# Kernel optimization log

Hardware: AMD Instinct MI355X
Metric: run time of the kernel (lower is better)

Reference implementation:

```python
import jax, jax.numpy as jnp
import numpy as np

B, H, S, D = 4, 16, 2048, 64

def setup_inputs() -> dict:
    key = jax.random.key(0)
    kq, kk, kv = jax.random.split(key, 3)
    q = jax.random.normal(kq, (B, H, S, D), dtype=jnp.float32)
    k = jax.random.normal(kk, (B, H, S, D), dtype=jnp.float32)
    v = jax.random.normal(kv, (B, H, S, D), dtype=jnp.float32)
    return {"q": q, "k": k, "v": v}

def reference(q, k, v):
    # naive unfused attention: scores = QK^T / sqrt(d), softmax, then @ V
    scale = 1.0 / jnp.sqrt(jnp.asarray(q.shape[-1], q.dtype))
    scores = jnp.einsum('bhqd,bhkd->bhqk', q, k) * scale  # [B,H,S,S] materialized
    attn = jax.nn.softmax(scores, axis=-1)
    out = jnp.einsum('bhqk,bhkd->bhqd', attn, v)
    return out
```

## Files before the change

kernel.cpp:

```cpp
#include <hip/hip_runtime.h>


#define S_LEN 2048
#define D_DIM 64
#define N_BH  64
#define QSCALE 0.18033688011112042f

typedef _Float16 half8 __attribute__((ext_vector_type(8)));
typedef _Float16 half4 __attribute__((ext_vector_type(4)));
typedef float floatx16 __attribute__((ext_vector_type(16)));
typedef unsigned int uint4v __attribute__((ext_vector_type(4)));

#define MFMA32(a, b, c) __builtin_amdgcn_mfma_f32_32x32x16_f16((a), (b), (c), 0, 0, 0)

#define GLL16(g, l) __builtin_amdgcn_global_load_lds(                      \
    (const __attribute__((address_space(1))) void*)(g),                    \
    (__attribute__((address_space(3))) void*)(l), 16, 0, 0)

__global__ __launch_bounds__(256) void prep_kernel(
    const float* __restrict__ kg, const float* __restrict__ vg,
    _Float16* __restrict__ kh, _Float16* __restrict__ vt)
{
    __shared__ _Float16 Ls[64 * 64];
    const int tid = threadIdx.x;
    const int bh = blockIdx.y;
    const int sbase = blockIdx.x * 64;
    const size_t gbase = ((size_t)(bh * S_LEN + sbase)) * D_DIM;

#pragma unroll
    for (int i = 0; i < 4; ++i) {
        const int e = i * 1024 + tid * 4;
        const int s = e >> 6, d0 = e & 63;
        const float4 kv = *(const float4*)(kg + gbase + e);
        half4 hk;
        hk[0] = (_Float16)kv.x; hk[1] = (_Float16)kv.y;
        hk[2] = (_Float16)kv.z; hk[3] = (_Float16)kv.w;
        *(half4*)(kh + gbase + e) = hk;
        const float4 vv = *(const float4*)(vg + gbase + e);
        const int base = ((((s >> 3) ^ ((d0 >> 2) & 7)) << 3) | (s & 7));
        Ls[(d0 + 0) * 64 + base] = (_Float16)vv.x;
        Ls[(d0 + 1) * 64 + base] = (_Float16)vv.y;
        Ls[(d0 + 2) * 64 + base] = (_Float16)vv.z;
        Ls[(d0 + 3) * 64 + base] = (_Float16)vv.w;
    }
    __syncthreads();
    const int d = tid >> 2, c = tid & 3, sw = (d >> 2) & 7;
    _Float16* dst = vt + ((size_t)(bh * D_DIM + d)) * S_LEN + sbase + c * 16;
    *(half8*)(dst)     = *(const half8*)&Ls[d * 64 + (((2 * c)     ^ sw) << 3)];
    *(half8*)(dst + 8) = *(const half8*)&Ls[d * 64 + (((2 * c + 1) ^ sw) << 3)];
}

__global__ __launch_bounds__(128) void fa_kernel(
    const float* __restrict__ qg, const _Float16* __restrict__ kh,
    const _Float16* __restrict__ vt, float* __restrict__ outg)
{
    __shared__ _Float16 Kl[64 * 64];
    __shared__ _Float16 Vl[64 * 64];

    const int tid = threadIdx.x;
    const int w = tid >> 6;
    const int L = tid & 63;
    const int lq = L & 31;
    const int h = L >> 5;

    const int id = blockIdx.x;
    const int bh   = ((id & 7) << 3) | (id >> 8);
    const int qblk = (id >> 3) & 31;
    const int qrow = qblk * 64 + w * 32 + lq;

    half8 qb[4];
    {
        const float* qp = qg + ((size_t)bh * S_LEN + qrow) * D_DIM + h * 8;
#pragma unroll
        for (int ks = 0; ks < 4; ++ks) {
            const float4 a = *(const float4*)(qp + ks * 16);
            const float4 b = *(const float4*)(qp + ks * 16 + 4);
            qb[ks][0] = (_Float16)(a.x * QSCALE);
            qb[ks][1] = (_Float16)(a.y * QSCALE);
            qb[ks][2] = (_Float16)(a.z * QSCALE);
            qb[ks][3] = (_Float16)(a.w * QSCALE);
            qb[ks][4] = (_Float16)(b.x * QSCALE);
            qb[ks][5] = (_Float16)(b.y * QSCALE);
            qb[ks][6] = (_Float16)(b.z * QSCALE);
            qb[ks][7] = (_Float16)(b.w * QSCALE);
        }
    }

    floatx16 o0, o1, lac;
#pragma unroll
    for (int r = 0; r < 16; ++r) { o0[r] = 0.f; o1[r] = 0.f; lac[r] = 0.f; }

    half8 ones;
#pragma unroll
    for (int j = 0; j < 8; ++j) ones[j] = (_Float16)1.0f;

    const int rloc = L >> 3, lc = L & 7;
    const int crd = lc ^ rloc;
    const _Float16* kgl = kh + (size_t)bh * S_LEN * D_DIM
                        + (size_t)(w * 32 + rloc) * D_DIM + crd * 8;
    const _Float16* vgl = vt + (size_t)bh * D_DIM * S_LEN
                        + (size_t)(w * 32 + rloc) * S_LEN + crd * 8;
    _Float16* const kld = &Kl[w * 32 * 64];
    _Float16* const vld = &Vl[w * 32 * 64];

    for (int kt = 0; kt < S_LEN / 64; ++kt) {
        __syncthreads();
#pragma unroll
        for (int i = 0; i < 4; ++i) {
            GLL16(kgl + (size_t)i * 8 * D_DIM, kld + i * 8 * 64);
            GLL16(vgl + (size_t)i * 8 * S_LEN, vld + i * 8 * 64);
        }
        kgl += 64 * D_DIM;
        vgl += 64;
        __syncthreads();

        floatx16 sa0, sa1;
#pragma unroll
        for (int r = 0; r < 16; ++r) { sa0[r] = 0.f; sa1[r] = 0.f; }
#pragma unroll
        for (int ks = 0; ks < 4; ++ks) {
            const int sw = (((2 * ks + h) ^ (lq & 7)) << 3);
            const half8 ka0 = *(const half8*)&Kl[lq * 64 + sw];
            const half8 ka1 = *(const half8*)&Kl[(32 + lq) * 64 + sw];
            sa0 = MFMA32(ka0, qb[ks], sa0);
            sa1 = MFMA32(ka1, qb[ks], sa1);
        }

        unsigned int pk0[8], pk1[8];
#pragma unroll
        for (int p = 0; p < 8; ++p) {
            const auto e0 = __builtin_amdgcn_cvt_pkrtz(
                __builtin_amdgcn_exp2f(sa0[2 * p]),
                __builtin_amdgcn_exp2f(sa0[2 * p + 1]));
            const auto e1 = __builtin_amdgcn_cvt_pkrtz(
                __builtin_amdgcn_exp2f(sa1[2 * p]),
                __builtin_amdgcn_exp2f(sa1[2 * p + 1]));
            pk0[p] = __builtin_bit_cast(unsigned int, e0);
            pk1[p] = __builtin_bit_cast(unsigned int, e1);
        }

#pragma unroll
        for (int mt = 0; mt < 2; ++mt) {
            const unsigned int* pk = mt ? pk1 : pk0;
            const unsigned int t0 = h ? pk[0] : pk[2];
            const unsigned int t1 = h ? pk[1] : pk[3];
            const unsigned int t2 = h ? pk[4] : pk[6];
            const unsigned int t3 = h ? pk[5] : pk[7];
            const unsigned int r0 = __shfl_xor(t0, 32, 64);
            const unsigned int r1 = __shfl_xor(t1, 32, 64);
            const unsigned int r2 = __shfl_xor(t2, 32, 64);
            const unsigned int r3 = __shfl_xor(t3, 32, 64);
            uint4v u0, u1;
            if (h == 0) {
                u0[0] = pk[0]; u0[1] = pk[1]; u0[2] = r0; u0[3] = r1;
                u1[0] = pk[4]; u1[1] = pk[5]; u1[2] = r2; u1[3] = r3;
            } else {
                u0[0] = r0; u0[1] = r1; u0[2] = pk[2]; u0[3] = pk[3];
                u1[0] = r2; u1[1] = r3; u1[2] = pk[6]; u1[3] = pk[7];
            }
            const half8 af0 = __builtin_bit_cast(half8, u0);
            const half8 af1 = __builtin_bit_cast(half8, u1);
#pragma unroll
            for (int kl = 0; kl < 2; ++kl) {
                const int ksg = mt * 2 + kl;
                const half8 af = kl ? af1 : af0;
                const int sw = (((2 * ksg + h) ^ (lq & 7)) << 3);
                const half8 vb0 = *(const half8*)&Vl[lq * 64 + sw];
                const half8 vb1 = *(const half8*)&Vl[(32 + lq) * 64 + sw];
                lac = MFMA32(af, ones, lac);
                o0 = MFMA32(af, vb0, o0);
                o1 = MFMA32(af, vb1, o1);
            }
        }
    }

    float* ob = outg + ((size_t)bh * S_LEN + qblk * 64 + w * 32) * D_DIM;
#pragma unroll
    for (int reg = 0; reg < 16; ++reg) {
        const int q = (reg & 3) + 8 * (reg >> 2) + 4 * h;
        const float inv = 1.0f / lac[reg];
        ob[(size_t)q * D_DIM + lq]      = o0[reg] * inv;
        ob[(size_t)q * D_DIM + 32 + lq] = o1[reg] * inv;
    }
}

extern "C" void kernel_launch(void* const* d_in, const int* in_sizes, int n_in,
                              void* d_out, int out_size, void* d_ws, size_t ws_size,
                              hipStream_t stream) {
    const float* q = (const float*)d_in[0];
    const float* k = (const float*)d_in[1];
    const float* v = (const float*)d_in[2];
    float* out = (float*)d_out;
    (void)in_sizes; (void)n_in; (void)out_size; (void)ws_size;

    _Float16* kh = (_Float16*)d_ws;
    _Float16* vt = kh + (size_t)N_BH * S_LEN * D_DIM;

    prep_kernel<<<dim3(S_LEN / 64, N_BH), dim3(256), 0, stream>>>(k, v, kh, vt);
    fa_kernel<<<dim3(2048), dim3(128), 0, stream>>>(q, kh, vt, out);
}
```

Before: 246.5 us.

## Process two query tiles per wave and halve row-sum MFMAs

Each wave now computes 64 query rows as two 32-row tiles, so every K and V fragment read from LDS feeds twice as many MFMAs. The block grows to 4 waves covering 256 query rows, and the grid shrinks to 512 blocks. The softmax denominator now takes one MFMA against a ones vector on the fp16 sum of the two P fragments, instead of two MFMAs. In exchange, register pressure roughly doubles, fewer waves are resident per CU, and the row sums are accumulated partly in fp16.

```diff
diff --git a/kernel.cpp b/kernel.cpp
--- a/kernel.cpp
+++ b/kernel.cpp
@@ -8,6 +8,7 @@
 
 typedef _Float16 half8 __attribute__((ext_vector_type(8)));
 typedef _Float16 half4 __attribute__((ext_vector_type(4)));
+typedef _Float16 half2v __attribute__((ext_vector_type(2)));
 typedef float floatx16 __attribute__((ext_vector_type(16)));
 typedef unsigned int uint4v __attribute__((ext_vector_type(4)));
 
@@ -50,7 +51,7 @@
     *(half8*)(dst + 8) = *(const half8*)&Ls[d * 64 + (((2 * c + 1) ^ sw) << 3)];
 }
 
-__global__ __launch_bounds__(128) void fa_kernel(
+__global__ __launch_bounds__(256) void fa_kernel(
     const float* __restrict__ qg, const _Float16* __restrict__ kh,
     const _Float16* __restrict__ vt, float* __restrict__ outg)
 {
@@ -64,31 +65,34 @@
     const int h = L >> 5;
 
     const int id = blockIdx.x;
-    const int bh   = ((id & 7) << 3) | (id >> 8);
-    const int qblk = (id >> 3) & 31;
-    const int qrow = qblk * 64 + w * 32 + lq;
-
-    half8 qb[4];
-    {
-        const float* qp = qg + ((size_t)bh * S_LEN + qrow) * D_DIM + h * 8;
+    const int bh   = ((id & 7) << 3) | (id >> 6);
+    const int qblk = (id >> 3) & 7;
+    const int qrow0 = qblk * 256 + w * 64 + lq;
+
+    half8 qb[2][4];
+#pragma unroll
+    for (int t = 0; t < 2; ++t) {
+        const float* qp = qg + ((size_t)bh * S_LEN + qrow0 + t * 32) * D_DIM + h * 8;
 #pragma unroll
         for (int ks = 0; ks < 4; ++ks) {
             const float4 a = *(const float4*)(qp + ks * 16);
             const float4 b = *(const float4*)(qp + ks * 16 + 4);
-            qb[ks][0] = (_Float16)(a.x * QSCALE);
-            qb[ks][1] = (_Float16)(a.y * QSCALE);
-            qb[ks][2] = (_Float16)(a.z * QSCALE);
-            qb[ks][3] = (_Float16)(a.w * QSCALE);
-            qb[ks][4] = (_Float16)(b.x * QSCALE);
-            qb[ks][5] = (_Float16)(b.y * QSCALE);
-            qb[ks][6] = (_Float16)(b.z * QSCALE);
-            qb[ks][7] = (_Float16)(b.w * QSCALE);
-        }
-    }
-
-    floatx16 o0, o1, lac;
-#pragma unroll
-    for (int r = 0; r < 16; ++r) { o0[r] = 0.f; o1[r] = 0.f; lac[r] = 0.f; }
+            qb[t][ks][0] = (_Float16)(a.x * QSCALE);
+            qb[t][ks][1] = (_Float16)(a.y * QSCALE);
+            qb[t][ks][2] = (_Float16)(a.z * QSCALE);
+            qb[t][ks][3] = (_Float16)(a.w * QSCALE);
+            qb[t][ks][4] = (_Float16)(b.x * QSCALE);
+            qb[t][ks][5] = (_Float16)(b.y * QSCALE);
+            qb[t][ks][6] = (_Float16)(b.z * QSCALE);
+            qb[t][ks][7] = (_Float16)(b.w * QSCALE);
+        }
+    }
+
+    floatx16 o0[2], o1[2], lac[2];
+#pragma unroll
+    for (int t = 0; t < 2; ++t)
+#pragma unroll
+        for (int r = 0; r < 16; ++r) { o0[t][r] = 0.f; o1[t][r] = 0.f; lac[t][r] = 0.f; }
 
     half8 ones;
 #pragma unroll
@@ -97,16 +101,16 @@
     const int rloc = L >> 3, lc = L & 7;
     const int crd = lc ^ rloc;
     const _Float16* kgl = kh + (size_t)bh * S_LEN * D_DIM
-                        + (size_t)(w * 32 + rloc) * D_DIM + crd * 8;
+                        + (size_t)(w * 16 + rloc) * D_DIM + crd * 8;
     const _Float16* vgl = vt + (size_t)bh * D_DIM * S_LEN
-                        + (size_t)(w * 32 + rloc) * S_LEN + crd * 8;
-    _Float16* const kld = &Kl[w * 32 * 64];
-    _Float16* const vld = &Vl[w * 32 * 64];
+                        + (size_t)(w * 16 + rloc) * S_LEN + crd * 8;
+    _Float16* const kld = &Kl[w * 16 * 64];
+    _Float16* const vld = &Vl[w * 16 * 64];
 
     for (int kt = 0; kt < S_LEN / 64; ++kt) {
         __syncthreads();
 #pragma unroll
-        for (int i = 0; i < 4; ++i) {
+        for (int i = 0; i < 2; ++i) {
             GLL16(kgl + (size_t)i * 8 * D_DIM, kld + i * 8 * 64);
             GLL16(vgl + (size_t)i * 8 * S_LEN, vld + i * 8 * 64);
         }
@@ -114,73 +118,90 @@
         vgl += 64;
         __syncthreads();
 
-        floatx16 sa0, sa1;
-#pragma unroll
-        for (int r = 0; r < 16; ++r) { sa0[r] = 0.f; sa1[r] = 0.f; }
+        floatx16 sa0[2], sa1[2];
+#pragma unroll
+        for (int t = 0; t < 2; ++t)
+#pragma unroll
+            for (int r = 0; r < 16; ++r) { sa0[t][r] = 0.f; sa1[t][r] = 0.f; }
 #pragma unroll
         for (int ks = 0; ks < 4; ++ks) {
             const int sw = (((2 * ks + h) ^ (lq & 7)) << 3);
             const half8 ka0 = *(const half8*)&Kl[lq * 64 + sw];
             const half8 ka1 = *(const half8*)&Kl[(32 + lq) * 64 + sw];
-            sa0 = MFMA32(ka0, qb[ks], sa0);
-            sa1 = MFMA32(ka1, qb[ks], sa1);
-        }
-
-        unsigned int pk0[8], pk1[8];
-#pragma unroll
-        for (int p = 0; p < 8; ++p) {
-            const auto e0 = __builtin_amdgcn_cvt_pkrtz(
-                __builtin_amdgcn_exp2f(sa0[2 * p]),
-                __builtin_amdgcn_exp2f(sa0[2 * p + 1]));
-            const auto e1 = __builtin_amdgcn_cvt_pkrtz(
-                __builtin_amdgcn_exp2f(sa1[2 * p]),
-                __builtin_amdgcn_exp2f(sa1[2 * p + 1]));
-            pk0[p] = __builtin_bit_cast(unsigned int, e0);
-            pk1[p] = __builtin_bit_cast(unsigned int, e1);
-        }
+            sa0[0] = MFMA32(ka0, qb[0][ks], sa0[0]);
+            sa1[0] = MFMA32(ka1, qb[0][ks], sa1[0]);
+            sa0[1] = MFMA32(ka0, qb[1][ks], sa0[1]);
+            sa1[1] = MFMA32(ka1, qb[1][ks], sa1[1]);
+        }
+
+        unsigned int pk0[2][8], pk1[2][8];
+#pragma unroll
+        for (int t = 0; t < 2; ++t)
+#pragma unroll
+            for (int p = 0; p < 8; ++p) {
+                const auto e0 = __builtin_amdgcn_cvt_pkrtz(
+                    __builtin_amdgcn_exp2f(sa0[t][2 * p]),
+                    __builtin_amdgcn_exp2f(sa0[t][2 * p + 1]));
+                const auto e1 = __builtin_amdgcn_cvt_pkrtz(
+                    __builtin_amdgcn_exp2f(sa1[t][2 * p]),
+                    __builtin_amdgcn_exp2f(sa1[t][2 * p + 1]));
+                pk0[t][p] = __builtin_bit_cast(unsigned int, e0);
+                pk1[t][p] = __builtin_bit_cast(unsigned int, e1);
+            }
 
 #pragma unroll
         for (int mt = 0; mt < 2; ++mt) {
-            const unsigned int* pk = mt ? pk1 : pk0;
-            const unsigned int t0 = h ? pk[0] : pk[2];
-            const unsigned int t1 = h ? pk[1] : pk[3];
-            const unsigned int t2 = h ? pk[4] : pk[6];
-            const unsigned int t3 = h ? pk[5] : pk[7];
-            const unsigned int r0 = __shfl_xor(t0, 32, 64);
-            const unsigned int r1 = __shfl_xor(t1, 32, 64);
-            const unsigned int r2 = __shfl_xor(t2, 32, 64);
-            const unsigned int r3 = __shfl_xor(t3, 32, 64);
-            uint4v u0, u1;
-            if (h == 0) {
-                u0[0] = pk[0]; u0[1] = pk[1]; u0[2] = r0; u0[3] = r1;
-                u1[0] = pk[4]; u1[1] = pk[5]; u1[2] = r2; u1[3] = r3;
-            } else {
-                u0[0] = r0; u0[1] = r1; u0[2] = pk[2]; u0[3] = pk[3];
-                u1[0] = r2; u1[1] = r3; u1[2] = pk[6]; u1[3] = pk[7];
+            half8 af0[2], af1[2];
+#pragma unroll
+            for (int t = 0; t < 2; ++t) {
+                const unsigned int* pk = mt ? pk1[t] : pk0[t];
+                const unsigned int t0 = h ? pk[0] : pk[2];
+                const unsigned int t1 = h ? pk[1] : pk[3];
+                const unsigned int t2 = h ? pk[4] : pk[6];
+                const unsigned int t3 = h ? pk[5] : pk[7];
+                const unsigned int r0 = __shfl_xor(t0, 32, 64);
+                const unsigned int r1 = __shfl_xor(t1, 32, 64);
+                const unsigned int r2 = __shfl_xor(t2, 32, 64);
+                const unsigned int r3 = __shfl_xor(t3, 32, 64);
+                uint4v u0, u1;
+                if (h == 0) {
+                    u0[0] = pk[0]; u0[1] = pk[1]; u0[2] = r0; u0[3] = r1;
+                    u1[0] = pk[4]; u1[1] = pk[5]; u1[2] = r2; u1[3] = r3;
+                } else {
+                    u0[0] = r0; u0[1] = r1; u0[2] = pk[2]; u0[3] = pk[3];
+                    u1[0] = r2; u1[1] = r3; u1[2] = pk[6]; u1[3] = pk[7];
+                }
+                af0[t] = __builtin_bit_cast(half8, u0);
+                af1[t] = __builtin_bit_cast(half8, u1);
+                const half8 afs = af0[t] + af1[t];
+                lac[t] = MFMA32(afs, ones, lac[t]);
             }
-            const half8 af0 = __builtin_bit_cast(half8, u0);
-            const half8 af1 = __builtin_bit_cast(half8, u1);
 #pragma unroll
             for (int kl = 0; kl < 2; ++kl) {
                 const int ksg = mt * 2 + kl;
-                const half8 af = kl ? af1 : af0;
                 const int sw = (((2 * ksg + h) ^ (lq & 7)) << 3);
                 const half8 vb0 = *(const half8*)&Vl[lq * 64 + sw];
                 const half8 vb1 = *(const half8*)&Vl[(32 + lq) * 64 + sw];
-                lac = MFMA32(af, ones, lac);
-                o0 = MFMA32(af, vb0, o0);
-                o1 = MFMA32(af, vb1, o1);
+#pragma unroll
+                for (int t = 0; t < 2; ++t) {
+                    const half8 af = kl ? af1[t] : af0[t];
+                    o0[t] = MFMA32(af, vb0, o0[t]);
+                    o1[t] = MFMA32(af, vb1, o1[t]);
+                }
             }
         }
     }
 
-    float* ob = outg + ((size_t)bh * S_LEN + qblk * 64 + w * 32) * D_DIM;
-#pragma unroll
-    for (int reg = 0; reg < 16; ++reg) {
-        const int q = (reg & 3) + 8 * (reg >> 2) + 4 * h;
-        const float inv = 1.0f / lac[reg];
-        ob[(size_t)q * D_DIM + lq]      = o0[reg] * inv;
-        ob[(size_t)q * D_DIM + 32 + lq] = o1[reg] * inv;
+#pragma unroll
+    for (int t = 0; t < 2; ++t) {
+        float* ob = outg + ((size_t)bh * S_LEN + qblk * 256 + w * 64 + t * 32) * D_DIM;
+#pragma unroll
+        for (int reg = 0; reg < 16; ++reg) {
+            const int q = (reg & 3) + 8 * (reg >> 2) + 4 * h;
+            const float inv = 1.0f / lac[t][reg];
+            ob[(size_t)q * D_DIM + lq]      = o0[t][reg] * inv;
+            ob[(size_t)q * D_DIM + 32 + lq] = o1[t][reg] * inv;
+        }
     }
 }
 
@@ -197,5 +218,5 @@
     _Float16* vt = kh + (size_t)N_BH * S_LEN * D_DIM;
 
     prep_kernel<<<dim3(S_LEN / 64, N_BH), dim3(256), 0, stream>>>(k, v, kh, vt);
-    fa_kernel<<<dim3(2048), dim3(128), 0, stream>>>(q, kh, vt, out);
+    fa_kernel<<<dim3(512), dim3(256), 0, stream>>>(q, kh, vt, out);
 }
```

After: 253.4 us. 1.03x slower.
